# Optimization experiments

Measured on AMD Instinct MI355X. Metric: run time of the kernel, lower is better.

Reference implementation:

```python
import jax, jax.numpy as jnp
import numpy as np


def setup_inputs() -> dict:
    key = jax.random.key(0)
    k1, k2 = jax.random.split(key)
    shape = (16, 64, 32, 28, 28)  # (b, c, t, h, w)
    x = jax.random.normal(k1, shape, dtype=jnp.float32)
    x_v = jax.random.normal(k2, shape, dtype=jnp.float32)
    return {"x": x, "x_v": x_v}


def reference(x, x_v):
    b, c, t, h, w = x.shape
    d = c * h * w
    # (b, t, d): flatten channel+spatial into feature dim per frame
    r_q = jnp.transpose(x, (0, 2, 1, 3, 4)).reshape(b, t, d)
    r_v = jnp.transpose(x_v, (0, 2, 1, 3, 4)).reshape(b, t, d)
    # (b, t, t) frame-frame similarity
    m_t = jnp.einsum('bqd,bkd->bqk', r_q, r_q)
    # NOTE: softmax over the BATCH axis (dim=0), faithful to the original
    m_t = jax.nn.softmax(m_t, axis=0)
    a_t = jnp.einsum('bqk,bkd->bqd', m_t, r_v)
    a = a_t.reshape(b, t, c, h, w).transpose(0, 2, 1, 3, 4)
    return a
```

## Files before the change

### kernel.cpp

```cpp
#include <hip/hip_runtime.h>

namespace {

constexpr int Tt = 32;
constexpr int Ss = 784;

using bf16x8 = __attribute__((ext_vector_type(8))) short;
using f32x4  = __attribute__((ext_vector_type(4))) float;

__device__ inline void cvt2(float a, float b, unsigned& h, unsigned& l) {
  const unsigned ha = __float_as_uint(a) >> 16;
  const unsigned hb = __float_as_uint(b) >> 16;
  const float ra = a - __uint_as_float(ha << 16);
  const float rb = b - __uint_as_float(hb << 16);
  const unsigned la = __float_as_uint(ra) >> 16;
  const unsigned lb = __float_as_uint(rb) >> 16;
  h = ha | (hb << 16);
  l = la | (lb << 16);
}

__global__ __launch_bounds__(256, 3) void gram_partial(const float* __restrict__ x,
                                                       float* __restrict__ part) {
  const int bc = blockIdx.x;
  const float* __restrict__ xb = x + (size_t)bc * (Tt * Ss);
  const int tid  = threadIdx.x;
  const int w    = tid >> 6;
  const int lane = tid & 63;

  __shared__ uint4 HI[13 * 128];
  __shared__ uint4 LO[13 * 128];

  f32x4 d1[2][2], d2[2][2], d3[2][2];
#pragma unroll
  for (int i = 0; i < 2; ++i)
#pragma unroll
    for (int j = 0; j < 2; ++j) { d1[i][j] = 0.f; d2[i][j] = 0.f; d3[i][j] = 0.f; }

  const int fbase = ((lane >> 4) << 5) + (lane & 15);

#pragma unroll
  for (int phase = 0; phase < 2; ++phase) {
    const int sb  = phase ? 416 : 0;
    const int nks = phase ? 12 : 13;

    for (int f = tid; f < nks * 128; f += 256) {
      const int ks  = f >> 7;
      const int idx = f & 127;
      const int kg  = idx >> 5;
      const int row = idx & 31;
      const int s   = sb + ks * 32 + kg * 8;
      uint4 h = {0u, 0u, 0u, 0u}, l = {0u, 0u, 0u, 0u};
      if (s < 784) {
        const float* p = xb + row * Ss + s;
        const float4 v0 = *reinterpret_cast<const float4*>(p);
        const float4 v1 = *reinterpret_cast<const float4*>(p + 4);
        cvt2(v0.x, v0.y, h.x, l.x);
        cvt2(v0.z, v0.w, h.y, l.y);
        cvt2(v1.x, v1.y, h.z, l.z);
        cvt2(v1.z, v1.w, h.w, l.w);
      }
      HI[f] = h;
      LO[f] = l;
    }
    __syncthreads();

    for (int ks = w; ks < nks; ks += 4) {
      const int base = ks * 128 + fbase;
      const uint4 h0u = HI[base], h1u = HI[base + 16];
      const uint4 l0u = LO[base], l1u = LO[base + 16];
      const bf16x8 h0 = __builtin_bit_cast(bf16x8, h0u);
      const bf16x8 h1 = __builtin_bit_cast(bf16x8, h1u);
      const bf16x8 l0 = __builtin_bit_cast(bf16x8, l0u);
      const bf16x8 l1 = __builtin_bit_cast(bf16x8, l1u);
      d1[0][0] = __builtin_amdgcn_mfma_f32_16x16x32_bf16(h0, h0, d1[0][0], 0, 0, 0);
      d1[0][1] = __builtin_amdgcn_mfma_f32_16x16x32_bf16(h0, h1, d1[0][1], 0, 0, 0);
      d1[1][0] = __builtin_amdgcn_mfma_f32_16x16x32_bf16(h1, h0, d1[1][0], 0, 0, 0);
      d1[1][1] = __builtin_amdgcn_mfma_f32_16x16x32_bf16(h1, h1, d1[1][1], 0, 0, 0);
      d2[0][0] = __builtin_amdgcn_mfma_f32_16x16x32_bf16(h0, l0, d2[0][0], 0, 0, 0);
      d2[0][1] = __builtin_amdgcn_mfma_f32_16x16x32_bf16(h0, l1, d2[0][1], 0, 0, 0);
      d2[1][0] = __builtin_amdgcn_mfma_f32_16x16x32_bf16(h1, l0, d2[1][0], 0, 0, 0);
      d2[1][1] = __builtin_amdgcn_mfma_f32_16x16x32_bf16(h1, l1, d2[1][1], 0, 0, 0);
      d3[0][0] = __builtin_amdgcn_mfma_f32_16x16x32_bf16(l0, h0, d3[0][0], 0, 0, 0);
      d3[0][1] = __builtin_amdgcn_mfma_f32_16x16x32_bf16(l0, h1, d3[0][1], 0, 0, 0);
      d3[1][0] = __builtin_amdgcn_mfma_f32_16x16x32_bf16(l1, h0, d3[1][0], 0, 0, 0);
      d3[1][1] = __builtin_amdgcn_mfma_f32_16x16x32_bf16(l1, h1, d3[1][1], 0, 0, 0);
    }
    __syncthreads();
  }

  float* mtmp = reinterpret_cast<float*>(HI);
#pragma unroll
  for (int i = 0; i < 2; ++i)
#pragma unroll
    for (int j = 0; j < 2; ++j) {
      const f32x4 s4 = d1[i][j] + d2[i][j] + d3[i][j];
#pragma unroll
      for (int r = 0; r < 4; ++r) {
        const int row = i * 16 + ((lane >> 4) << 2) + r;
        const int col = j * 16 + (lane & 15);
        mtmp[w * 1056 + row * 33 + col] = s4[r];
      }
    }
  __syncthreads();

  const int e0 = tid * 4;
  float tmp[4];
#pragma unroll
  for (int u = 0; u < 4; ++u) {
    const int row = (e0 + u) >> 5;
    const int col = (e0 + u) & 31;
    float ss = 0.f;
#pragma unroll
    for (int ww = 0; ww < 4; ++ww) ss += mtmp[ww * 1056 + row * 33 + col];
    tmp[u] = ss;
  }
  float4 o4;
  o4.x = tmp[0]; o4.y = tmp[1]; o4.z = tmp[2]; o4.w = tmp[3];
  *reinterpret_cast<float4*>(part + (size_t)bc * 1024 + e0) = o4;
}

__global__ __launch_bounds__(256) void reduce_c(const float* __restrict__ part,
                                                float* __restrict__ msum) {
  const int bid = blockIdx.x;
  const int b   = bid >> 2;
  const int e   = (bid & 3) * 256 + threadIdx.x;
  const float* __restrict__ p = part + (size_t)b * 64 * 1024 + e;
  float s0 = 0.f, s1 = 0.f, s2 = 0.f, s3 = 0.f;
#pragma unroll
  for (int c = 0; c < 64; c += 4) {
    s0 += p[(size_t)(c + 0) * 1024];
    s1 += p[(size_t)(c + 1) * 1024];
    s2 += p[(size_t)(c + 2) * 1024];
    s3 += p[(size_t)(c + 3) * 1024];
  }
  msum[b * 1024 + e] = (s0 + s1) + (s2 + s3);
}

__global__ __launch_bounds__(256) void softmax_b(const float* __restrict__ msum,
                                                 float* __restrict__ mq) {
  const int e = blockIdx.x * 256 + threadIdx.x;
  float l[16];
  float mx = -3.4e38f;
#pragma unroll
  for (int b = 0; b < 16; ++b) {
    l[b] = msum[b * 1024 + e];
    mx = fmaxf(mx, l[b]);
  }
  float s = 0.f;
#pragma unroll
  for (int b = 0; b < 16; ++b) {
    l[b] = expf(l[b] - mx);
    s += l[b];
  }
  const float inv = 1.f / s;
#pragma unroll
  for (int b = 0; b < 16; ++b) mq[b * 1024 + e] = l[b] * inv;
}

__global__ __launch_bounds__(256, 4) void pv(const float* __restrict__ xv,
                                             const float* __restrict__ mq,
                                             float* __restrict__ out) {
  const int bc = blockIdx.x;
  const int b  = bc >> 6;
  const float* __restrict__ xvb = xv + (size_t)bc * (Tt * Ss);
  float* __restrict__ ob        = out + (size_t)bc * (Tt * Ss);

  const int tid  = threadIdx.x;
  const int w    = tid >> 6;
  const int lane = tid & 63;
  const int col  = lane & 15;
  const int g    = lane >> 4;

  __shared__ float lds[32 * 257];

  bf16x8 mh[2], ml[2];
#pragma unroll
  for (int qf = 0; qf < 2; ++qf) {
    const float* mp = mq + b * 1024 + (qf * 16 + col) * 32 + g * 8;
    const float4 ma = *reinterpret_cast<const float4*>(mp);
    const float4 mb = *reinterpret_cast<const float4*>(mp + 4);
    uint4 h, l;
    cvt2(ma.x, ma.y, h.x, l.x);
    cvt2(ma.z, ma.w, h.y, l.y);
    cvt2(mb.x, mb.y, h.z, l.z);
    cvt2(mb.z, mb.w, h.w, l.w);
    mh[qf] = __builtin_bit_cast(bf16x8, h);
    ml[qf] = __builtin_bit_cast(bf16x8, l);
  }

  for (int ch = 0; ch < 3; ++ch) {
#pragma unroll
    for (int it = 0; it < 8; ++it) {
      const int v   = it * 256 + tid;
      const int c8  = v & 7;
      const int row = (v >> 3) & 31;
      const int c4  = ((v >> 8) << 3) + c8;
      const float4 x4 = *reinterpret_cast<const float4*>(xvb + row * Ss + ch * 256 + c4 * 4);
      float* d = &lds[row * 257 + c4 * 4];
      d[0] = x4.x; d[1] = x4.y; d[2] = x4.z; d[3] = x4.w;
    }
    __syncthreads();

#pragma unroll
    for (int sfi = 0; sfi < 4; ++sfi) {
      const int sf = w + sfi * 4;
      float f8[8];
#pragma unroll
      for (int j = 0; j < 8; ++j) f8[j] = lds[(g * 8 + j) * 257 + sf * 16 + col];
      uint4 hh, lv;
      cvt2(f8[0], f8[1], hh.x, lv.x);
      cvt2(f8[2], f8[3], hh.y, lv.y);
      cvt2(f8[4], f8[5], hh.z, lv.z);
      cvt2(f8[6], f8[7], hh.w, lv.w);
      const bf16x8 vh = __builtin_bit_cast(bf16x8, hh);
      const bf16x8 vl = __builtin_bit_cast(bf16x8, lv);
      const int s = ch * 256 + sf * 16 + col;
#pragma unroll
      for (int qf = 0; qf < 2; ++qf) {
        f32x4 d = {0.f, 0.f, 0.f, 0.f};
        d = __builtin_amdgcn_mfma_f32_16x16x32_bf16(mh[qf], vl, d, 0, 0, 0);
        d = __builtin_amdgcn_mfma_f32_16x16x32_bf16(ml[qf], vh, d, 0, 0, 0);
        d = __builtin_amdgcn_mfma_f32_16x16x32_bf16(mh[qf], vh, d, 0, 0, 0);
#pragma unroll
        for (int r = 0; r < 4; ++r)
          ob[(size_t)(qf * 16 + g * 4 + r) * Ss + s] = d[r];
      }
    }
    __syncthreads();
  }

  if (w == 0) {
    float f8[8];
#pragma unroll
    for (int j = 0; j < 8; ++j) f8[j] = xvb[(size_t)(g * 8 + j) * Ss + 768 + col];
    uint4 hh, lv;
    cvt2(f8[0], f8[1], hh.x, lv.x);
    cvt2(f8[2], f8[3], hh.y, lv.y);
    cvt2(f8[4], f8[5], hh.z, lv.z);
    cvt2(f8[6], f8[7], hh.w, lv.w);
    const bf16x8 vh = __builtin_bit_cast(bf16x8, hh);
    const bf16x8 vl = __builtin_bit_cast(bf16x8, lv);
    const int s = 768 + col;
#pragma unroll
    for (int qf = 0; qf < 2; ++qf) {
      f32x4 d = {0.f, 0.f, 0.f, 0.f};
      d = __builtin_amdgcn_mfma_f32_16x16x32_bf16(mh[qf], vl, d, 0, 0, 0);
      d = __builtin_amdgcn_mfma_f32_16x16x32_bf16(ml[qf], vh, d, 0, 0, 0);
      d = __builtin_amdgcn_mfma_f32_16x16x32_bf16(mh[qf], vh, d, 0, 0, 0);
#pragma unroll
      for (int r = 0; r < 4; ++r)
        ob[(size_t)(qf * 16 + g * 4 + r) * Ss + s] = d[r];
    }
  }
}

}

extern "C" void kernel_launch(void* const* d_in, const int* in_sizes, int n_in,
                              void* d_out, int out_size, void* d_ws, size_t ws_size,
                              hipStream_t stream) {
  const float* x  = (const float*)d_in[0];
  const float* xv = (const float*)d_in[1];
  float* out = (float*)d_out;

  float* part = (float*)d_ws;
  float* msum = part + 1024 * 1024;
  float* mq   = msum + 16 * 1024;

  gram_partial<<<dim3(1024), dim3(256), 0, stream>>>(x, part);
  reduce_c<<<dim3(64), dim3(256), 0, stream>>>(part, msum);
  softmax_b<<<dim3(4), dim3(256), 0, stream>>>(msum, mq);
  pv<<<dim3(1024), dim3(256), 0, stream>>>(xv, mq, out);
}
```

Before: 87.45 us.

## Load Gram and PV MFMA operands directly from global memory, drop LDS staging

In gram_partial, each wave now loads its fragment rows straight from global memory into registers, does the bf16 hi/lo split there and feeds MFMA. This removes the LDS HI/LO staging buffers and the barriers between phases, and the occupancy hint rises from 3 to 4 blocks. In pv, the LDS tile and barriers are likewise removed: each wave handles 12 contiguous 16-column fragments (wave 3 takes one extra) by reading global memory directly. The cost is less coalesced, strided global loads (8 rows per lane, 16 contiguous floats per row) in place of cooperative float4 staging.

```diff
diff --git a/kernel.cpp b/kernel.cpp
--- a/kernel.cpp
+++ b/kernel.cpp
@@ -19,16 +19,15 @@
   l = la | (lb << 16);
 }
 
-__global__ __launch_bounds__(256, 3) void gram_partial(const float* __restrict__ x,
+__global__ __launch_bounds__(256, 4) void gram_partial(const float* __restrict__ x,
                                                        float* __restrict__ part) {
   const int bc = blockIdx.x;
   const float* __restrict__ xb = x + (size_t)bc * (Tt * Ss);
   const int tid  = threadIdx.x;
   const int w    = tid >> 6;
   const int lane = tid & 63;
-
-  __shared__ uint4 HI[13 * 128];
-  __shared__ uint4 LO[13 * 128];
+  const int col  = lane & 15;
+  const int g    = lane >> 4;
 
   f32x4 d1[2][2], d2[2][2], d3[2][2];
 #pragma unroll
@@ -36,59 +35,46 @@
 #pragma unroll
     for (int j = 0; j < 2; ++j) { d1[i][j] = 0.f; d2[i][j] = 0.f; d3[i][j] = 0.f; }
 
-  const int fbase = ((lane >> 4) << 5) + (lane & 15);
-
-#pragma unroll
-  for (int phase = 0; phase < 2; ++phase) {
-    const int sb  = phase ? 416 : 0;
-    const int nks = phase ? 12 : 13;
-
-    for (int f = tid; f < nks * 128; f += 256) {
-      const int ks  = f >> 7;
-      const int idx = f & 127;
-      const int kg  = idx >> 5;
-      const int row = idx & 31;
-      const int s   = sb + ks * 32 + kg * 8;
-      uint4 h = {0u, 0u, 0u, 0u}, l = {0u, 0u, 0u, 0u};
-      if (s < 784) {
-        const float* p = xb + row * Ss + s;
-        const float4 v0 = *reinterpret_cast<const float4*>(p);
-        const float4 v1 = *reinterpret_cast<const float4*>(p + 4);
-        cvt2(v0.x, v0.y, h.x, l.x);
-        cvt2(v0.z, v0.w, h.y, l.y);
-        cvt2(v1.x, v1.y, h.z, l.z);
-        cvt2(v1.z, v1.w, h.w, l.w);
-      }
-      HI[f] = h;
-      LO[f] = l;
+  const float* __restrict__ pa = xb + (size_t)col * Ss;
+  const float* __restrict__ pb = xb + (size_t)(16 + col) * Ss;
+
+  for (int ks = w; ks < 25; ks += 4) {
+    const int s0 = ks * 32 + g * 8;
+    uint4 ha = {0u,0u,0u,0u}, la = {0u,0u,0u,0u};
+    uint4 hb = {0u,0u,0u,0u}, lb = {0u,0u,0u,0u};
+    if (s0 < 784) {
+      const float4 a0 = *reinterpret_cast<const float4*>(pa + s0);
+      const float4 a1 = *reinterpret_cast<const float4*>(pa + s0 + 4);
+      const float4 b0 = *reinterpret_cast<const float4*>(pb + s0);
+      const float4 b1 = *reinterpret_cast<const float4*>(pb + s0 + 4);
+      cvt2(a0.x, a0.y, ha.x, la.x);
+      cvt2(a0.z, a0.w, ha.y, la.y);
+      cvt2(a1.x, a1.y, ha.z, la.z);
+      cvt2(a1.z, a1.w, ha.w, la.w);
+      cvt2(b0.x, b0.y, hb.x, lb.x);
+      cvt2(b0.z, b0.w, hb.y, lb.y);
+      cvt2(b1.x, b1.y, hb.z, lb.z);
+      cvt2(b1.z, b1.w, hb.w, lb.w);
     }
-    __syncthreads();
-
-    for (int ks = w; ks < nks; ks += 4) {
-      const int base = ks * 128 + fbase;
-      const uint4 h0u = HI[base], h1u = HI[base + 16];
-      const uint4 l0u = LO[base], l1u = LO[base + 16];
-      const bf16x8 h0 = __builtin_bit_cast(bf16x8, h0u);
-      const bf16x8 h1 = __builtin_bit_cast(bf16x8, h1u);
-      const bf16x8 l0 = __builtin_bit_cast(bf16x8, l0u);
-      const bf16x8 l1 = __builtin_bit_cast(bf16x8, l1u);
-      d1[0][0] = __builtin_amdgcn_mfma_f32_16x16x32_bf16(h0, h0, d1[0][0], 0, 0, 0);
-      d1[0][1] = __builtin_amdgcn_mfma_f32_16x16x32_bf16(h0, h1, d1[0][1], 0, 0, 0);
-      d1[1][0] = __builtin_amdgcn_mfma_f32_16x16x32_bf16(h1, h0, d1[1][0], 0, 0, 0);
-      d1[1][1] = __builtin_amdgcn_mfma_f32_16x16x32_bf16(h1, h1, d1[1][1], 0, 0, 0);
-      d2[0][0] = __builtin_amdgcn_mfma_f32_16x16x32_bf16(h0, l0, d2[0][0], 0, 0, 0);
-      d2[0][1] = __builtin_amdgcn_mfma_f32_16x16x32_bf16(h0, l1, d2[0][1], 0, 0, 0);
-      d2[1][0] = __builtin_amdgcn_mfma_f32_16x16x32_bf16(h1, l0, d2[1][0], 0, 0, 0);
-      d2[1][1] = __builtin_amdgcn_mfma_f32_16x16x32_bf16(h1, l1, d2[1][1], 0, 0, 0);
-      d3[0][0] = __builtin_amdgcn_mfma_f32_16x16x32_bf16(l0, h0, d3[0][0], 0, 0, 0);
-      d3[0][1] = __builtin_amdgcn_mfma_f32_16x16x32_bf16(l0, h1, d3[0][1], 0, 0, 0);
-      d3[1][0] = __builtin_amdgcn_mfma_f32_16x16x32_bf16(l1, h0, d3[1][0], 0, 0, 0);
-      d3[1][1] = __builtin_amdgcn_mfma_f32_16x16x32_bf16(l1, h1, d3[1][1], 0, 0, 0);
-    }
-    __syncthreads();
-  }
-
-  float* mtmp = reinterpret_cast<float*>(HI);
+    const bf16x8 h0 = __builtin_bit_cast(bf16x8, ha);
+    const bf16x8 l0 = __builtin_bit_cast(bf16x8, la);
+    const bf16x8 h1 = __builtin_bit_cast(bf16x8, hb);
+    const bf16x8 l1 = __builtin_bit_cast(bf16x8, lb);
+    d1[0][0] = __builtin_amdgcn_mfma_f32_16x16x32_bf16(h0, h0, d1[0][0], 0, 0, 0);
+    d1[0][1] = __builtin_amdgcn_mfma_f32_16x16x32_bf16(h0, h1, d1[0][1], 0, 0, 0);
+    d1[1][0] = __builtin_amdgcn_mfma_f32_16x16x32_bf16(h1, h0, d1[1][0], 0, 0, 0);
+    d1[1][1] = __builtin_amdgcn_mfma_f32_16x16x32_bf16(h1, h1, d1[1][1], 0, 0, 0);
+    d2[0][0] = __builtin_amdgcn_mfma_f32_16x16x32_bf16(h0, l0, d2[0][0], 0, 0, 0);
+    d2[0][1] = __builtin_amdgcn_mfma_f32_16x16x32_bf16(h0, l1, d2[0][1], 0, 0, 0);
+    d2[1][0] = __builtin_amdgcn_mfma_f32_16x16x32_bf16(h1, l0, d2[1][0], 0, 0, 0);
+    d2[1][1] = __builtin_amdgcn_mfma_f32_16x16x32_bf16(h1, l1, d2[1][1], 0, 0, 0);
+    d3[0][0] = __builtin_amdgcn_mfma_f32_16x16x32_bf16(l0, h0, d3[0][0], 0, 0, 0);
+    d3[0][1] = __builtin_amdgcn_mfma_f32_16x16x32_bf16(l0, h1, d3[0][1], 0, 0, 0);
+    d3[1][0] = __builtin_amdgcn_mfma_f32_16x16x32_bf16(l1, h0, d3[1][0], 0, 0, 0);
+    d3[1][1] = __builtin_amdgcn_mfma_f32_16x16x32_bf16(l1, h1, d3[1][1], 0, 0, 0);
+  }
+
+  __shared__ float mtmp[4 * 1056];
 #pragma unroll
   for (int i = 0; i < 2; ++i)
 #pragma unroll
@@ -96,9 +82,9 @@
       const f32x4 s4 = d1[i][j] + d2[i][j] + d3[i][j];
 #pragma unroll
       for (int r = 0; r < 4; ++r) {
-        const int row = i * 16 + ((lane >> 4) << 2) + r;
-        const int col = j * 16 + (lane & 15);
-        mtmp[w * 1056 + row * 33 + col] = s4[r];
+        const int row = i * 16 + g * 4 + r;
+        const int cc  = j * 16 + col;
+        mtmp[w * 1056 + row * 33 + cc] = s4[r];
       }
     }
   __syncthreads();
@@ -108,10 +94,10 @@
 #pragma unroll
   for (int u = 0; u < 4; ++u) {
     const int row = (e0 + u) >> 5;
-    const int col = (e0 + u) & 31;
+    const int cc  = (e0 + u) & 31;
     float ss = 0.f;
 #pragma unroll
-    for (int ww = 0; ww < 4; ++ww) ss += mtmp[ww * 1056 + row * 33 + col];
+    for (int ww = 0; ww < 4; ++ww) ss += mtmp[ww * 1056 + row * 33 + cc];
     tmp[u] = ss;
   }
   float4 o4;
@@ -170,8 +156,6 @@
   const int lane = tid & 63;
   const int col  = lane & 15;
   const int g    = lane >> 4;
-
-  __shared__ float lds[32 * 257];
 
   bf16x8 mh[2], ml[2];
 #pragma unroll
@@ -188,51 +172,11 @@
     ml[qf] = __builtin_bit_cast(bf16x8, l);
   }
 
-  for (int ch = 0; ch < 3; ++ch) {
-#pragma unroll
-    for (int it = 0; it < 8; ++it) {
-      const int v   = it * 256 + tid;
-      const int c8  = v & 7;
-      const int row = (v >> 3) & 31;
-      const int c4  = ((v >> 8) << 3) + c8;
-      const float4 x4 = *reinterpret_cast<const float4*>(xvb + row * Ss + ch * 256 + c4 * 4);
-      float* d = &lds[row * 257 + c4 * 4];
-      d[0] = x4.x; d[1] = x4.y; d[2] = x4.z; d[3] = x4.w;
-    }
-    __syncthreads();
-
-#pragma unroll
-    for (int sfi = 0; sfi < 4; ++sfi) {
-      const int sf = w + sfi * 4;
-      float f8[8];
-#pragma unroll
-      for (int j = 0; j < 8; ++j) f8[j] = lds[(g * 8 + j) * 257 + sf * 16 + col];
-      uint4 hh, lv;
-      cvt2(f8[0], f8[1], hh.x, lv.x);
-      cvt2(f8[2], f8[3], hh.y, lv.y);
-      cvt2(f8[4], f8[5], hh.z, lv.z);
-      cvt2(f8[6], f8[7], hh.w, lv.w);
-      const bf16x8 vh = __builtin_bit_cast(bf16x8, hh);
-      const bf16x8 vl = __builtin_bit_cast(bf16x8, lv);
-      const int s = ch * 256 + sf * 16 + col;
-#pragma unroll
-      for (int qf = 0; qf < 2; ++qf) {
-        f32x4 d = {0.f, 0.f, 0.f, 0.f};
-        d = __builtin_amdgcn_mfma_f32_16x16x32_bf16(mh[qf], vl, d, 0, 0, 0);
-        d = __builtin_amdgcn_mfma_f32_16x16x32_bf16(ml[qf], vh, d, 0, 0, 0);
-        d = __builtin_amdgcn_mfma_f32_16x16x32_bf16(mh[qf], vh, d, 0, 0, 0);
-#pragma unroll
-        for (int r = 0; r < 4; ++r)
-          ob[(size_t)(qf * 16 + g * 4 + r) * Ss + s] = d[r];
-      }
-    }
-    __syncthreads();
-  }
-
-  if (w == 0) {
+  auto do_frag = [&](int sf) {
     float f8[8];
 #pragma unroll
-    for (int j = 0; j < 8; ++j) f8[j] = xvb[(size_t)(g * 8 + j) * Ss + 768 + col];
+    for (int j = 0; j < 8; ++j)
+      f8[j] = xvb[(size_t)(8 * g + j) * Ss + sf * 16 + col];
     uint4 hh, lv;
     cvt2(f8[0], f8[1], hh.x, lv.x);
     cvt2(f8[2], f8[3], hh.y, lv.y);
@@ -240,7 +184,7 @@
     cvt2(f8[6], f8[7], hh.w, lv.w);
     const bf16x8 vh = __builtin_bit_cast(bf16x8, hh);
     const bf16x8 vl = __builtin_bit_cast(bf16x8, lv);
-    const int s = 768 + col;
+    const int s = sf * 16 + col;
 #pragma unroll
     for (int qf = 0; qf < 2; ++qf) {
       f32x4 d = {0.f, 0.f, 0.f, 0.f};
@@ -251,7 +195,12 @@
       for (int r = 0; r < 4; ++r)
         ob[(size_t)(qf * 16 + g * 4 + r) * Ss + s] = d[r];
     }
-  }
+  };
+
+  const int f0 = w * 12;
+#pragma unroll
+  for (int i = 0; i < 12; ++i) do_frag(f0 + i);
+  if (w == 3) do_frag(48);
 }
 
 }
```

Result: slower. 95.43 us (+9.1%).
